# Kernel optimization log

Hardware: AMD Instinct MI355X
Metric: run time of the kernel (lower is better)

Reference implementation:

```python
import jax, jax.numpy as jnp
import numpy as np

DIM = 1024
HEADS = 16
HEAD_DIM = DIM // HEADS
B, N = 512, 65
EPS = 1e-5


def layernorm(x, w, b):
    # LayerNorm over last dim (head_dim), eps matching torch default
    mu = jnp.mean(x, axis=-1, keepdims=True)
    var = jnp.var(x, axis=-1, keepdims=True)
    return (x - mu) * jax.lax.rsqrt(var + EPS) * w + b


def setup_inputs() -> dict:
    key = jax.random.key(0)
    ks = jax.random.split(key, 8)
    s = 0.02
    return {
        "x": jax.random.normal(ks[0], (B, N, DIM), dtype=jnp.float32),
        "w_qkv": jax.random.normal(ks[1], (3 * DIM, DIM), dtype=jnp.float32) * s,
        "w_proj": jax.random.normal(ks[2], (DIM, DIM), dtype=jnp.float32) * s,
        "qn_w": jnp.ones((HEAD_DIM,), jnp.float32),
        "qn_b": jnp.zeros((HEAD_DIM,), jnp.float32),
        "kn_w": jnp.ones((HEAD_DIM,), jnp.float32),
        "kn_b": jnp.zeros((HEAD_DIM,), jnp.float32),
        "bias": jax.random.normal(ks[3], (HEADS, 65, 65), dtype=jnp.float32) * 0.1,
        "bias_scale": jnp.array(1.0, jnp.float32),
    }


def reference(x, w_qkv, w_proj, qn_w, qn_b, kn_w, kn_b, bias, bias_scale):
    Bsz, n, C = x.shape
    scale = HEAD_DIM ** -0.5
    qkv = jnp.einsum('bnc,dc->bnd', x, w_qkv)              # [B,N,3C]
    qkv = qkv.reshape(Bsz, n, 3, HEADS, HEAD_DIM)
    qkv = jnp.transpose(qkv, (2, 0, 3, 1, 4))              # [3,B,H,N,hd]
    q, k, v = qkv[0], qkv[1], qkv[2]
    q = layernorm(q, qn_w, qn_b) * scale
    k = layernorm(k, kn_w, kn_b)
    attn = jnp.einsum('bhnd,bhmd->bhnm', q, k)             # [B,H,N,N]
    attn = attn + (bias[:, :n, :n] * bias_scale)[None]
    attn = jax.nn.softmax(attn, axis=-1)
    out = jnp.einsum('bhnm,bhmd->bhnd', attn, v)           # [B,H,N,hd]
    out = jnp.transpose(out, (0, 2, 1, 3)).reshape(Bsz, n, C)
    return jnp.einsum('bnc,dc->bnd', out, w_proj)
```

## Files before the change

### kernel.cpp

```cpp
#include <hip/hip_runtime.h>
#include <stdint.h>

#define HEADS 16
#define BSZ 512
#define NTOK 65
#define MTOK (BSZ * NTOK)
#define NX  34078720UL
#define NQW 3145728UL
#define NPW 1048576UL

typedef __attribute__((ext_vector_type(8))) short bf16x8;
typedef __attribute__((ext_vector_type(4))) float f32x4;

__device__ __forceinline__ unsigned short f2bf(float f) {
  unsigned u = __float_as_uint(f);
  u += 0x7FFFu + ((u >> 16) & 1u);
  return (unsigned short)(u >> 16);
}

__global__ __launch_bounds__(256) void cast3_kernel(
    const float* __restrict__ x, const float* __restrict__ wq, const float* __restrict__ wp,
    unsigned short* __restrict__ xb, unsigned short* __restrict__ wqb, unsigned short* __restrict__ wpb) {
  size_t u = ((size_t)blockIdx.x * 256 + threadIdx.x) * 4;
  const float* src; unsigned short* dst; size_t off;
  if (u < NX)            { src = x;  dst = xb;  off = u; }
  else if (u < NX + NQW) { src = wq; dst = wqb; off = u - NX; }
  else                   { src = wp; dst = wpb; off = u - NX - NQW; }
  float4 v = *(const float4*)(src + off);
  ushort4 o;
  o.x = f2bf(v.x); o.y = f2bf(v.y); o.z = f2bf(v.z); o.w = f2bf(v.w);
  *(ushort4*)(dst + off) = o;
}

template <int MODE, int NBN>
__global__ __launch_bounds__(512, 2) void gemm256_kernel(
    const unsigned short* __restrict__ A, const unsigned short* __restrict__ Bm,
    unsigned short* __restrict__ qws, unsigned short* __restrict__ kws,
    unsigned short* __restrict__ vws, float* __restrict__ outp,
    const float* __restrict__ qn_w, const float* __restrict__ qn_b,
    const float* __restrict__ kn_w, const float* __restrict__ kn_b) {
  __shared__ unsigned short As0[256 * 64];
  __shared__ unsigned short Bs0[256 * 64];
  __shared__ unsigned short As1[256 * 64];
  __shared__ unsigned short Bs1[256 * 64];
  const int tid = threadIdx.x;
  const int wid = tid >> 6, lane = tid & 63;
  const int lrow = lane & 15, lk = lane >> 4;
  const int wm = wid >> 2, wn = wid & 3;

  const int chunk = (int)gridDim.x >> 3;
  const int orig = blockIdx.x;
  const int wg = (orig & 7) * chunk + (orig >> 3);
  const int bm = wg / NBN, bn = wg - bm * NBN;

  const size_t arow0 = (size_t)bm * 256, brow0 = (size_t)bn * 256;

  const unsigned short* pA[4];
  const unsigned short* pB[4];
  int dstc[4];
#pragma unroll
  for (int j = 0; j < 4; ++j) {
    int ci = j * 512 + tid;
    int row = ci >> 3;
    int k8 = (ci & 7) ^ (row & 7);
    pA[j] = A + (arow0 + row) * 1024 + k8 * 8;
    pB[j] = Bm + (brow0 + row) * 1024 + k8 * 8;
    dstc[j] = (j * 512 + wid * 64) * 4;
  }

  f32x4 acc[2][4][4] = {};

  auto stage = [&](unsigned short* __restrict__ dA, unsigned short* __restrict__ dB, int ktn) {
    const int koff = ktn * 64;
#pragma unroll
    for (int j = 0; j < 4; ++j) {
      __builtin_amdgcn_global_load_lds(
          (const __attribute__((address_space(1))) unsigned int*)(pA[j] + koff),
          (__attribute__((address_space(3))) unsigned int*)dA + dstc[j], 16, 0, 0);
      __builtin_amdgcn_global_load_lds(
          (const __attribute__((address_space(1))) unsigned int*)(pB[j] + koff),
          (__attribute__((address_space(3))) unsigned int*)dB + dstc[j], 16, 0, 0);
    }
  };

  auto ktile = [&](const unsigned short* __restrict__ RA, const unsigned short* __restrict__ RB,
                   unsigned short* __restrict__ WA, unsigned short* __restrict__ WB, int ktn) {
    if (ktn < 16) stage(WA, WB, ktn);
#pragma unroll
    for (int kk = 0; kk < 2; ++kk) {
      const int cpos8 = ((kk * 4 + lk) ^ (lrow & 7)) * 8;
      bf16x8 bv[4];
#pragma unroll
      for (int nt = 0; nt < 4; ++nt)
        bv[nt] = *(const bf16x8*)&RB[(wn * 64 + nt * 16 + lrow) * 64 + cpos8];
#pragma unroll
      for (int mh = 0; mh < 2; ++mh) {
        bf16x8 av[4];
#pragma unroll
        for (int mt = 0; mt < 4; ++mt)
          av[mt] = *(const bf16x8*)&RA[(wm * 128 + mh * 64 + mt * 16 + lrow) * 64 + cpos8];
        __builtin_amdgcn_s_barrier();
        __builtin_amdgcn_s_setprio(1);
#pragma unroll
        for (int mt = 0; mt < 4; ++mt)
#pragma unroll
          for (int nt = 0; nt < 4; ++nt)
            acc[mh][mt][nt] =
                __builtin_amdgcn_mfma_f32_16x16x32_bf16(av[mt], bv[nt], acc[mh][mt][nt], 0, 0, 0);
        __builtin_amdgcn_s_setprio(0);
      }
    }
    __syncthreads();
  };

  stage(As0, Bs0, 0);
  __syncthreads();

#pragma unroll 1
  for (int kt2 = 0; kt2 < 8; ++kt2) {
    ktile(As0, Bs0, As1, Bs1, 2 * kt2 + 1);
    ktile(As1, Bs1, As0, Bs0, 2 * kt2 + 2);
  }

  if (MODE == 0) {
    const int sec = bn >> 2;
    const int h0 = ((bn & 3) << 2) + wn;
    const float qsc = (sec == 0) ? 0.125f : 1.0f;
    float wv[4], bvv[4];
    if (sec < 2) {
      const float* wp_ = sec ? kn_w : qn_w;
      const float* bp_ = sec ? kn_b : qn_b;
#pragma unroll
      for (int nt = 0; nt < 4; ++nt) {
        wv[nt] = wp_[nt * 16 + lrow];
        bvv[nt] = bp_[nt * 16 + lrow];
      }
    }
    unsigned short* qk_dst = sec ? kws : qws;
#pragma unroll
    for (int mh = 0; mh < 2; ++mh)
#pragma unroll
      for (int mt = 0; mt < 4; ++mt)
#pragma unroll
        for (int r = 0; r < 4; ++r) {
          int grow = bm * 256 + wm * 128 + mh * 64 + mt * 16 + lk * 4 + r;
          int b = grow / 65, nn = grow - b * 65;
          int bh = b * HEADS + h0;
          if (sec < 2) {
            float s = 0.f, s2 = 0.f;
#pragma unroll
            for (int nt = 0; nt < 4; ++nt) {
              float f = acc[mh][mt][nt][r];
              s += f; s2 += f * f;
            }
            s += __shfl_xor(s, 1); s2 += __shfl_xor(s2, 1);
            s += __shfl_xor(s, 2); s2 += __shfl_xor(s2, 2);
            s += __shfl_xor(s, 4); s2 += __shfl_xor(s2, 4);
            s += __shfl_xor(s, 8); s2 += __shfl_xor(s2, 8);
            float mu = s * 0.015625f;
            float rstd = rsqrtf(s2 * 0.015625f - mu * mu + 1e-5f);
            size_t base = ((size_t)bh * 65 + nn) * 64;
#pragma unroll
            for (int nt = 0; nt < 4; ++nt)
              qk_dst[base + nt * 16 + lrow] =
                  f2bf(((acc[mh][mt][nt][r] - mu) * rstd * wv[nt] + bvv[nt]) * qsc);
          } else {
#pragma unroll
            for (int nt = 0; nt < 4; ++nt)
              vws[((size_t)bh * 64 + nt * 16 + lrow) * 80 + nn] = f2bf(acc[mh][mt][nt][r]);
          }
        }
  } else {
    const size_t cb = (size_t)bn * 256 + wn * 64 + lrow;
#pragma unroll
    for (int mh = 0; mh < 2; ++mh)
#pragma unroll
      for (int mt = 0; mt < 4; ++mt)
#pragma unroll
        for (int r = 0; r < 4; ++r) {
          float* rp = outp +
              (size_t)(bm * 256 + wm * 128 + mh * 64 + mt * 16 + lk * 4 + r) * 1024 + cb;
#pragma unroll
          for (int nt = 0; nt < 4; ++nt) rp[nt * 16] = acc[mh][mt][nt][r];
        }
  }
}

__global__ __launch_bounds__(320, 4) void attn_kernel(
    const unsigned short* __restrict__ qws, const unsigned short* __restrict__ kws,
    const unsigned short* __restrict__ vws,
    const float* __restrict__ bias, const float* __restrict__ bias_scale,
    unsigned short* __restrict__ aws) {
  __shared__ unsigned short qk_s[2 * 80 * 64];
  __shared__ unsigned short v_s[64 * 128];
  const int tid = threadIdx.x;
  const int wid = tid >> 6;
  const int bh = blockIdx.x;
  const int b = bh >> 4, h = bh & 15;
  const size_t qbase = (size_t)bh * 65 * 64;
  const size_t vbase = (size_t)bh * 64 * 80;

  {
    int ci = tid;
    int row = ci >> 3, k8 = (ci & 7) ^ (row & 7);
    __builtin_amdgcn_global_load_lds(
        (const __attribute__((address_space(1))) unsigned int*)(qws + qbase + row * 64 + k8 * 8),
        (__attribute__((address_space(3))) unsigned int*)qk_s + (size_t)(wid * 64) * 4,
        16, 0, 0);
    __builtin_amdgcn_global_load_lds(
        (const __attribute__((address_space(1))) unsigned int*)(kws + qbase + row * 64 + k8 * 8),
        (__attribute__((address_space(3))) unsigned int*)qk_s + (size_t)(640 + wid * 64) * 4,
        16, 0, 0);
  }
  if (wid < 3) {
    int ci = 320 + tid;
    int row = ci >> 3, k8 = (ci & 7) ^ (row & 7);
    __builtin_amdgcn_global_load_lds(
        (const __attribute__((address_space(1))) unsigned int*)(qws + qbase + row * 64 + k8 * 8),
        (__attribute__((address_space(3))) unsigned int*)qk_s + (size_t)(320 + wid * 64) * 4,
        16, 0, 0);
    __builtin_amdgcn_global_load_lds(
        (const __attribute__((address_space(1))) unsigned int*)(kws + qbase + row * 64 + k8 * 8),
        (__attribute__((address_space(3))) unsigned int*)qk_s + (size_t)(640 + 320 + wid * 64) * 4,
        16, 0, 0);
  }
  if (tid < 8) {
    bf16x8 tq = *(const bf16x8*)&qws[qbase + 64 * 64 + tid * 8];
    *(bf16x8*)&qk_s[64 * 64 + tid * 8] = tq;
  } else if (tid < 16) {
    int t = tid - 8;
    bf16x8 tk = *(const bf16x8*)&kws[qbase + 64 * 64 + t * 8];
    *(bf16x8*)&qk_s[5120 + 64 * 64 + t * 8] = tk;
  }
#pragma unroll
  for (int it = 0; it < 3; ++it) {
    int ci = it * 320 + tid;
    int d = ci >> 4, cs = ci & 15;
    int c = cs ^ (d & 7);
    __builtin_amdgcn_global_load_lds(
        (const __attribute__((address_space(1))) unsigned int*)(vws + vbase + d * 80 + c * 8),
        (__attribute__((address_space(3))) unsigned int*)v_s + (size_t)(it * 320 + wid * 64) * 4,
        16, 0, 0);
  }
  if (wid == 0) {
    int ci = 960 + tid;
    int d = ci >> 4, cs = ci & 15;
    int c = cs ^ (d & 7);
    __builtin_amdgcn_global_load_lds(
        (const __attribute__((address_space(1))) unsigned int*)(vws + vbase + d * 80 + c * 8),
        (__attribute__((address_space(3))) unsigned int*)v_s + (size_t)(960) * 4,
        16, 0, 0);
  }
  __syncthreads();

  const int lane = tid & 63;
  const int lrow = lane & 15, lk = lane >> 4;
  const float bsc = *bias_scale;
  const unsigned short* q_s = qk_s;
  const unsigned short* k_s = qk_s + 5120;
  unsigned short* p_s = qk_s;
  const int s = wid;

  unsigned int pk[5][2];
  {
    f32x4 accs[5] = {};
#pragma unroll
    for (int kk = 0; kk < 2; ++kk) {
      const int cpos = (kk * 4 + lk) ^ (lrow & 7);
      bf16x8 af = *(const bf16x8*)&q_s[(s * 16 + lrow) * 64 + cpos * 8];
#pragma unroll
      for (int nt = 0; nt < 5; ++nt) {
        bf16x8 bv = *(const bf16x8*)&k_s[(nt * 16 + lrow) * 64 + cpos * 8];
        accs[nt] = __builtin_amdgcn_mfma_f32_16x16x32_bf16(af, bv, accs[nt], 0, 0, 0);
      }
    }
#pragma unroll
    for (int r = 0; r < 4; ++r) {
      int row = s * 16 + lk * 4 + r;
      int brow = row > 64 ? 64 : row;
      float vals[5];
#pragma unroll
      for (int nt = 0; nt < 5; ++nt) {
        int col = nt * 16 + lrow;
        float v = accs[nt][r];
        if (col < 65) v += bias[((size_t)h * 65 + brow) * 65 + col] * bsc;
        else v = -1e30f;
        vals[nt] = v;
      }
      float m = vals[0];
#pragma unroll
      for (int nt = 1; nt < 5; ++nt) m = fmaxf(m, vals[nt]);
      m = fmaxf(m, __shfl_xor(m, 1)); m = fmaxf(m, __shfl_xor(m, 2));
      m = fmaxf(m, __shfl_xor(m, 4)); m = fmaxf(m, __shfl_xor(m, 8));
      float ssum = 0.f;
#pragma unroll
      for (int nt = 0; nt < 5; ++nt) { vals[nt] = __expf(vals[nt] - m); ssum += vals[nt]; }
      ssum += __shfl_xor(ssum, 1); ssum += __shfl_xor(ssum, 2);
      ssum += __shfl_xor(ssum, 4); ssum += __shfl_xor(ssum, 8);
      float inv = 1.0f / ssum;
#pragma unroll
      for (int nt = 0; nt < 5; ++nt) {
        unsigned int u = (unsigned int)f2bf(vals[nt] * inv);
        if ((r & 1) == 0) pk[nt][r >> 1] = u;
        else pk[nt][r >> 1] |= u << 16;
      }
    }
  }

  __syncthreads();

#pragma unroll
  for (int r = 0; r < 4; ++r) {
    int row = s * 16 + lk * 4 + r;
#pragma unroll
    for (int nt = 0; nt < 5; ++nt) {
      int col = nt * 16 + lrow;
      p_s[row * 128 + ((col >> 3) ^ (row & 7)) * 8 + (col & 7)] =
          (unsigned short)(pk[nt][r >> 1] >> ((r & 1) * 16));
    }
    {
      int col = 80 + lrow;
      p_s[row * 128 + ((col >> 3) ^ (row & 7)) * 8 + (col & 7)] = 0;
    }
  }
  __syncthreads();

  const size_t obase = (size_t)b * 65 * 1024 + h * 64;
  {
    f32x4 acco[4] = {};
#pragma unroll
    for (int kk = 0; kk < 3; ++kk) {
      const int cpos = (kk * 4 + lk) ^ (lrow & 7);
      bf16x8 af = *(const bf16x8*)&p_s[(s * 16 + lrow) * 128 + cpos * 8];
#pragma unroll
      for (int nt = 0; nt < 4; ++nt) {
        bf16x8 bv = *(const bf16x8*)&v_s[(nt * 16 + lrow) * 128 + cpos * 8];
        acco[nt] = __builtin_amdgcn_mfma_f32_16x16x32_bf16(af, bv, acco[nt], 0, 0, 0);
      }
    }
#pragma unroll
    for (int r = 0; r < 4; ++r) {
      int row = s * 16 + lk * 4 + r;
      if (row < 65) {
#pragma unroll
        for (int nt = 0; nt < 4; ++nt)
          aws[obase + (size_t)row * 1024 + nt * 16 + lrow] = f2bf(acco[nt][r]);
      }
    }
  }
}

extern "C" void kernel_launch(void* const* d_in, const int* in_sizes, int n_in,
                              void* d_out, int out_size, void* d_ws, size_t ws_size,
                              hipStream_t stream) {
  const float* x     = (const float*)d_in[0];
  const float* wqkv  = (const float*)d_in[1];
  const float* wproj = (const float*)d_in[2];
  const float* qn_w  = (const float*)d_in[3];
  const float* qn_b  = (const float*)d_in[4];
  const float* kn_w  = (const float*)d_in[5];
  const float* kn_b  = (const float*)d_in[6];
  const float* bias  = (const float*)d_in[7];
  const float* bsc   = (const float*)d_in[8];
  float* out = (float*)d_out;

  unsigned short* xb  = (unsigned short*)d_ws;
  unsigned short* wqb = xb + NX;
  unsigned short* wpb = wqb + NQW;
  unsigned short* qws = wpb + NPW;
  unsigned short* kws = qws + 34078720UL;
  unsigned short* vws = kws + 34078720UL;
  unsigned short* aws = vws + 41943040UL;

  cast3_kernel<<<37376, 256, 0, stream>>>(x, wqkv, wproj, xb, wqb, wpb);
  gemm256_kernel<0, 12><<<1560, 512, 0, stream>>>(xb, wqb, qws, kws, vws, nullptr,
                                                  qn_w, qn_b, kn_w, kn_b);
  attn_kernel<<<8192, 320, 0, stream>>>(qws, kws, vws, bias, bsc, aws);
  gemm256_kernel<1, 4><<<520, 512, 0, stream>>>(aws, wpb, nullptr, nullptr, nullptr, out,
                                                nullptr, nullptr, nullptr, nullptr);
}
```

Baseline: 733.3 us.

## Pipeline GEMM main loop with split-K half-tile staging and explicit vmcnt waits

Restructures the 256x256 bf16 GEMM main loop. LDS is reorganized into a single buffer split by k-halves of 32, with a new XOR swizzle. Global-to-LDS loads for later k-tiles are interleaved between the MFMA phases, and s_waitcnt vmcnt keeps loads in flight across tiles instead of draining at each __syncthreads. This aims to hide global memory latency behind compute, at the cost of more barriers per tile and fragile manual waitcnt accounting.

```diff
diff --git a/kernel.cpp b/kernel.cpp
--- a/kernel.cpp
+++ b/kernel.cpp
@@ -11,6 +11,8 @@
 
 typedef __attribute__((ext_vector_type(8))) short bf16x8;
 typedef __attribute__((ext_vector_type(4))) float f32x4;
+
+#define CFENCE asm volatile("" ::: "memory")
 
 __device__ __forceinline__ unsigned short f2bf(float f) {
   unsigned u = __float_as_uint(f);
@@ -39,10 +41,7 @@
     unsigned short* __restrict__ vws, float* __restrict__ outp,
     const float* __restrict__ qn_w, const float* __restrict__ qn_b,
     const float* __restrict__ kn_w, const float* __restrict__ kn_b) {
-  __shared__ unsigned short As0[256 * 64];
-  __shared__ unsigned short Bs0[256 * 64];
-  __shared__ unsigned short As1[256 * 64];
-  __shared__ unsigned short Bs1[256 * 64];
+  __shared__ unsigned short L[65536];
   const int tid = threadIdx.x;
   const int wid = tid >> 6, lane = tid & 63;
   const int lrow = lane & 15, lk = lane >> 4;
@@ -53,74 +52,99 @@
   const int wg = (orig & 7) * chunk + (orig >> 3);
   const int bm = wg / NBN, bn = wg - bm * NBN;
 
-  const size_t arow0 = (size_t)bm * 256, brow0 = (size_t)bn * 256;
-
-  const unsigned short* pA[4];
-  const unsigned short* pB[4];
-  int dstc[4];
-#pragma unroll
-  for (int j = 0; j < 4; ++j) {
+  const unsigned short* Abase = A + (size_t)bm * 256 * 1024;
+  const unsigned short* Bbase = Bm + (size_t)bn * 256 * 1024;
+
+  int srow[2], sk4x8[2], dstu[2];
+#pragma unroll
+  for (int j = 0; j < 2; ++j) {
     int ci = j * 512 + tid;
-    int row = ci >> 3;
-    int k8 = (ci & 7) ^ (row & 7);
-    pA[j] = A + (arow0 + row) * 1024 + k8 * 8;
-    pB[j] = Bm + (brow0 + row) * 1024 + k8 * 8;
-    dstc[j] = (j * 512 + wid * 64) * 4;
-  }
+    int row = ci >> 2, slot = ci & 3;
+    srow[j] = row;
+    sk4x8[j] = (slot ^ ((row >> 1) & 3)) * 8;
+    dstu[j] = (j * 512 + wid * 64) * 4;
+  }
+  const int cpos8 = (lk ^ ((lrow >> 1) & 3)) * 8;
 
   f32x4 acc[2][4][4] = {};
 
-  auto stage = [&](unsigned short* __restrict__ dA, unsigned short* __restrict__ dB, int ktn) {
-    const int koff = ktn * 64;
-#pragma unroll
-    for (int j = 0; j < 4; ++j) {
+  auto stageA = [&](int kk, int tau) {
+    const int baseu = (tau & 1) * 16384 + kk * 4096;
+#pragma unroll
+    for (int j = 0; j < 2; ++j)
       __builtin_amdgcn_global_load_lds(
-          (const __attribute__((address_space(1))) unsigned int*)(pA[j] + koff),
-          (__attribute__((address_space(3))) unsigned int*)dA + dstc[j], 16, 0, 0);
+          (const __attribute__((address_space(1))) unsigned int*)
+              (Abase + (size_t)srow[j] * 1024 + tau * 64 + kk * 32 + sk4x8[j]),
+          (__attribute__((address_space(3))) unsigned int*)L + baseu + dstu[j], 16, 0, 0);
+  };
+  auto stageB = [&](int kk, int tau) {
+    const int baseu = (tau & 1) * 16384 + 8192 + kk * 4096;
+#pragma unroll
+    for (int j = 0; j < 2; ++j)
       __builtin_amdgcn_global_load_lds(
-          (const __attribute__((address_space(1))) unsigned int*)(pB[j] + koff),
-          (__attribute__((address_space(3))) unsigned int*)dB + dstc[j], 16, 0, 0);
-    }
-  };
-
-  auto ktile = [&](const unsigned short* __restrict__ RA, const unsigned short* __restrict__ RB,
-                   unsigned short* __restrict__ WA, unsigned short* __restrict__ WB, int ktn) {
-    if (ktn < 16) stage(WA, WB, ktn);
-#pragma unroll
-    for (int kk = 0; kk < 2; ++kk) {
-      const int cpos8 = ((kk * 4 + lk) ^ (lrow & 7)) * 8;
-      bf16x8 bv[4];
+          (const __attribute__((address_space(1))) unsigned int*)
+              (Bbase + (size_t)srow[j] * 1024 + tau * 64 + kk * 32 + sk4x8[j]),
+          (__attribute__((address_space(3))) unsigned int*)L + baseu + dstu[j], 16, 0, 0);
+  };
+
+  auto rdB = [&](int t, int kk, bf16x8 (&bv)[4]) {
+    const int base = (t & 1) * 32768 + 16384 + kk * 8192 + cpos8;
+#pragma unroll
+    for (int nt = 0; nt < 4; ++nt)
+      bv[nt] = *(const bf16x8*)&L[base + (wn * 64 + nt * 16 + lrow) * 32];
+  };
+  auto rdA = [&](int t, int kk, int mh, bf16x8 (&av)[4]) {
+    const int base = (t & 1) * 32768 + kk * 8192 + cpos8;
+    const int r0 = wm * 128 + mh * 64;
+#pragma unroll
+    for (int mt = 0; mt < 4; ++mt)
+      av[mt] = *(const bf16x8*)&L[base + (r0 + mt * 16 + lrow) * 32];
+  };
+  auto mfma16 = [&](bf16x8 (&av)[4], bf16x8 (&bv)[4], f32x4 (&ac)[4][4]) {
+    __builtin_amdgcn_s_setprio(1);
+#pragma unroll
+    for (int mt = 0; mt < 4; ++mt)
 #pragma unroll
       for (int nt = 0; nt < 4; ++nt)
-        bv[nt] = *(const bf16x8*)&RB[(wn * 64 + nt * 16 + lrow) * 64 + cpos8];
-#pragma unroll
-      for (int mh = 0; mh < 2; ++mh) {
-        bf16x8 av[4];
-#pragma unroll
-        for (int mt = 0; mt < 4; ++mt)
-          av[mt] = *(const bf16x8*)&RA[(wm * 128 + mh * 64 + mt * 16 + lrow) * 64 + cpos8];
-        __builtin_amdgcn_s_barrier();
-        __builtin_amdgcn_s_setprio(1);
-#pragma unroll
-        for (int mt = 0; mt < 4; ++mt)
-#pragma unroll
-          for (int nt = 0; nt < 4; ++nt)
-            acc[mh][mt][nt] =
-                __builtin_amdgcn_mfma_f32_16x16x32_bf16(av[mt], bv[nt], acc[mh][mt][nt], 0, 0, 0);
-        __builtin_amdgcn_s_setprio(0);
-      }
-    }
-    __syncthreads();
-  };
-
-  stage(As0, Bs0, 0);
-  __syncthreads();
+        ac[mt][nt] = __builtin_amdgcn_mfma_f32_16x16x32_bf16(av[mt], bv[nt], ac[mt][nt], 0, 0, 0);
+    __builtin_amdgcn_s_setprio(0);
+  };
+
+  auto ktile = [&](int t, int st, int wc) {
+    bf16x8 bv[4], av[4];
+    rdB(t, 0, bv); rdA(t, 0, 0, av);
+    if (st & 1) stageA(1, t + 1);
+    CFENCE; __builtin_amdgcn_s_barrier(); CFENCE;
+    mfma16(av, bv, acc[0]);
+    CFENCE; __builtin_amdgcn_s_barrier(); CFENCE;
+    rdA(t, 0, 1, av);
+    if (st & 2) stageB(0, t + 2);
+    CFENCE; __builtin_amdgcn_s_barrier(); CFENCE;
+    mfma16(av, bv, acc[1]);
+    CFENCE; __builtin_amdgcn_s_barrier(); CFENCE;
+    rdB(t, 1, bv); rdA(t, 1, 0, av);
+    if (st & 4) stageA(0, t + 2);
+    CFENCE; __builtin_amdgcn_s_barrier(); CFENCE;
+    mfma16(av, bv, acc[0]);
+    CFENCE; __builtin_amdgcn_s_barrier(); CFENCE;
+    rdA(t, 1, 1, av);
+    if (st & 8) stageB(1, t + 2);
+    CFENCE; __builtin_amdgcn_s_barrier(); CFENCE;
+    mfma16(av, bv, acc[1]);
+    if (wc == 6)      asm volatile("s_waitcnt vmcnt(6)" ::: "memory");
+    else if (wc == 0) asm volatile("s_waitcnt vmcnt(0)" ::: "memory");
+    CFENCE; __builtin_amdgcn_s_barrier(); CFENCE;
+  };
+
+  stageB(0, 0); stageA(0, 0); stageB(1, 0); stageA(1, 0);
+  stageB(0, 1); stageA(0, 1); stageB(1, 1);
+  asm volatile("s_waitcnt vmcnt(6)" ::: "memory");
+  __builtin_amdgcn_s_barrier(); CFENCE;
 
 #pragma unroll 1
-  for (int kt2 = 0; kt2 < 8; ++kt2) {
-    ktile(As0, Bs0, As1, Bs1, 2 * kt2 + 1);
-    ktile(As1, Bs1, As0, Bs0, 2 * kt2 + 2);
-  }
+  for (int t = 0; t < 14; ++t) ktile(t, 0xF, 6);
+  ktile(14, 0x1, 0);
+  ktile(15, 0x0, -1);
 
   if (MODE == 0) {
     const int sec = bn >> 2;
```

New measurement: 729.4 us. About the same (-0.5%).
